# Kernel tuning notes

Hardware: AMD Instinct MI355X
Metric: run time of the kernel (lower is better)

Reference implementation:

```python
import jax, jax.numpy as jnp
import numpy as np

B, N, C_IN, T, K, C_OUT = 16, 1024, 64, 24, 3, 64


def setup_inputs() -> dict:
    key = jax.random.key(0)
    k1, k2, k3, k4 = jax.random.split(key, 4)
    x = jax.random.normal(k1, (B, N, C_IN, T), dtype=jnp.float32)
    STDG = jax.random.uniform(k2, (B, N, N), dtype=jnp.float32)
    cheb = jax.random.normal(k3, (K, N, N), dtype=jnp.float32)
    theta = jax.random.normal(k4, (K, C_IN, C_OUT), dtype=jnp.float32)
    return {"x": x, "STDG": STDG, "cheb": cheb, "theta": theta}


def reference(x, STDG, cheb, theta):
    # x: [B, N, C_in, T]; STDG: [B, N, N]; cheb: [K, N, N]; theta: [K, C_in, C_out]
    # original per (t, k): ((T_k * STDG).T @ x[..., t]) @ theta_k, summed over k, relu
    masked = cheb[:, None, :, :] * STDG[None]              # [K, B, N, N]
    # transpose of masked acts on node dim m: out_n = sum_m masked[k,b,m,n] * x[b,m,c,t]
    rhs = jnp.einsum('kbmn,bmct->kbnct', masked, x)        # [K, B, N, C_in, T]
    out = jnp.einsum('kbnct,kco->bnot', rhs, theta)        # [B, N, C_out, T]
    return jax.nn.relu(out)
```

## Files before the change

kernel.cpp:

```cpp
#include <hip/hip_runtime.h>
#include <stdint.h>


#define BB   16
#define NN   1024
#define CIN  64
#define TT   24
#define KCH  3
#define COUT 64
#define PP   (KCH*NN)
#define JJ   (COUT*TT)

typedef __attribute__((ext_vector_type(4))) float f32x4;
typedef __attribute__((ext_vector_type(8))) short bf16x8;

typedef __attribute__((address_space(1))) const unsigned int* gas_cuintp;
typedef __attribute__((address_space(3))) unsigned int* las_uintp;

static __device__ __forceinline__ unsigned short f2bf(float f){
  union { float f; unsigned u; } v; v.f = f;
  unsigned r = v.u + 0x7fffu + ((v.u >> 16) & 1u);
  return (unsigned short)(r >> 16);
}

__global__ __launch_bounds__(256) void kprepA(const float* __restrict__ cheb,
                                              const float* __restrict__ stdg,
                                              unsigned short* __restrict__ Ah,
                                              int b0){
  int nt = blockIdx.x;
  int mt = blockIdx.y;
  int bk = blockIdx.z;
  int bb = bk / 3, k = bk - bb * 3;
  int b = b0 + bb;
  __shared__ float alds[64][65];
  int tid = threadIdx.x;
  {
    int rm = tid >> 2;
    int nc = (tid & 3) << 4;
    const float* cp = cheb + ((size_t)(k*NN + mt*64 + rm))*NN + nt*64 + nc;
    const float* sp = stdg + ((size_t)(b*NN + mt*64 + rm))*NN + nt*64 + nc;
    #pragma unroll
    for (int i = 0; i < 16; i += 4){
      f32x4 cv = *(const f32x4*)(cp + i);
      f32x4 sv = *(const f32x4*)(sp + i);
      #pragma unroll
      for (int q = 0; q < 4; q++) alds[nc + i + q][rm] = cv[q] * sv[q];
    }
  }
  __syncthreads();
  {
    int rn = tid >> 2;
    int mc = (tid & 3) << 4;
    union { unsigned short s[16]; uint4 v[2]; } hb;
    #pragma unroll
    for (int i = 0; i < 16; i++) hb.s[i] = f2bf(alds[rn][mc + i]);
    size_t ob = ((size_t)(bb*NN + nt*64 + rn))*PP + (size_t)k*NN + mt*64 + mc;
    *(uint4*)(Ah + ob)     = hb.v[0];
    *(uint4*)(Ah + ob + 8) = hb.v[1];
  }
}

__global__ __launch_bounds__(256) void kprepY(const float* __restrict__ x,
                                              const float* __restrict__ theta,
                                              unsigned short* __restrict__ Yt,
                                              int b0){
  int jb = blockIdx.x;
  int ms = blockIdx.y;
  int bb = blockIdx.z;
  int b  = b0 + bb;
  __shared__ float xs[32*196];
  __shared__ float ths[3*64*8];
  __shared__ unsigned short ytile[192*32];
  int tid = threadIdx.x;
  int mi = tid >> 3, oi = tid & 7;

  for (int i = tid; i < 3*64*8; i += 256){
    int k = i >> 9, rem = i & 511;
    int c = rem >> 3, o = rem & 7;
    ths[i] = theta[k*(CIN*COUT) + c*COUT + jb*8 + o];
  }

  float acc0[24], acc1[24], acc2[24];
  #pragma unroll
  for (int t = 0; t < 24; t++){ acc0[t]=0.f; acc1[t]=0.f; acc2[t]=0.f; }

  const f32x4* xg4 = (const f32x4*)(x + ((size_t)(b*NN + ms*32))*CIN*TT);
  for (int cc = 0; cc < 8; cc++){
    __syncthreads();
    for (int i4 = tid; i4 < 32*48; i4 += 256){
      int m = i4 / 48, r = i4 - m*48;
      *(f32x4*)&xs[m*196 + r*4] = xg4[m*384 + cc*48 + r];
    }
    __syncthreads();
    for (int c8 = 0; c8 < 8; c8++){
      float xv[24];
      #pragma unroll
      for (int q = 0; q < 6; q++) *(f32x4*)&xv[q*4] = *(const f32x4*)&xs[mi*196 + c8*24 + q*4];
      int cg = cc*8 + c8;
      float t0 = ths[0*512 + cg*8 + oi];
      float t1 = ths[1*512 + cg*8 + oi];
      float t2 = ths[2*512 + cg*8 + oi];
      #pragma unroll
      for (int t = 0; t < 24; t++){
        acc0[t] = fmaf(t0, xv[t], acc0[t]);
        acc1[t] = fmaf(t1, xv[t], acc1[t]);
        acc2[t] = fmaf(t2, xv[t], acc2[t]);
      }
    }
  }

  #pragma unroll
  for (int k = 0; k < 3; k++){
    const float* a = (k==0) ? acc0 : (k==1) ? acc1 : acc2;
    __syncthreads();
    #pragma unroll
    for (int t = 0; t < 24; t++){
      int row = oi*24 + t;
      int sw  = (row >> 3) & 3;
      int sc  = (mi >> 3) ^ sw;
      ytile[row*32 + sc*8 + (mi & 7)] = f2bf(a[t]);
    }
    __syncthreads();
    for (int r = 0; r < 3; r++){
      int i   = tid + r*256;
      int row = i >> 2, c4 = i & 3;
      int sw  = (row >> 3) & 3;
      uint4 v = *(const uint4*)&ytile[row*32 + (c4 ^ sw)*8];
      size_t ob = ((size_t)bb*JJ + (size_t)jb*192 + row)*PP + k*NN + ms*32 + c4*8;
      *(uint4*)(Yt + ob) = v;
    }
  }
}

__global__ __launch_bounds__(256, 2) void kgemm(
    const unsigned short* __restrict__ Ah,
    const unsigned short* __restrict__ Yh,
    float* __restrict__ out, int b0){
  __shared__ unsigned short AsL[128*64];
  __shared__ unsigned short YsL[128*64];
  int orig = blockIdx.x;
  int cpx  = (int)(gridDim.x >> 3);
  int wgid = ((orig & 7) * cpx) + (orig >> 3);
  int bb  = wgid / 96;
  int r96 = wgid - bb*96;
  int nt  = r96 / 12;
  int jt  = r96 - nt*12;
  int tid = threadIdx.x;
  int lane = tid & 63, wave = tid >> 6;
  int wr = wave >> 1, wc = wave & 1;

  unsigned aoff[4], yoff[4];
  #pragma unroll
  for (int it = 0; it < 4; it++){
    int c = tid + it*256;
    int row = c >> 3;
    int sc = (c & 7) ^ (row & 7);
    aoff[it] = (unsigned)(((bb*NN + nt*128 + row) * PP) * 2 + sc * 16);
    yoff[it] = (unsigned)(((bb*JJ + jt*128 + row) * PP) * 2 + sc * 16);
  }

  f32x4 acc[4][4];
  #pragma unroll
  for (int i = 0; i < 4; i++)
    #pragma unroll
    for (int q = 0; q < 4; q++) acc[i][q] = (f32x4){0.f, 0.f, 0.f, 0.f};

  unsigned ldsw = (unsigned)(wave * 1024);
  const char* pA = (const char*)Ah;
  const char* pY = (const char*)Yh;

  for (int ps = 0; ps < PP/64; ps++){
    unsigned so = (unsigned)(ps * 128);
    #pragma unroll
    for (int it = 0; it < 4; it++){
      unsigned ld = ldsw + it*4096;
      __builtin_amdgcn_global_load_lds((gas_cuintp)(pA + aoff[it] + so), (las_uintp)((char*)AsL + ld), 16, 0, 0);
      __builtin_amdgcn_global_load_lds((gas_cuintp)(pY + yoff[it] + so), (las_uintp)((char*)YsL + ld), 16, 0, 0);
    }
    __syncthreads();
    #pragma unroll
    for (int kk = 0; kk < 2; kk++){
      bf16x8 a_f[4], y_f[4];
      #pragma unroll
      for (int i = 0; i < 4; i++){
        int arow = wr*64 + i*16 + (lane & 15);
        int ach  = ((kk*4) + (lane >> 4)) ^ (arow & 7);
        a_f[i] = *(const bf16x8*)&AsL[arow*64 + ach*8];
        int jrow = wc*64 + i*16 + (lane & 15);
        int jch  = ((kk*4) + (lane >> 4)) ^ (jrow & 7);
        y_f[i] = *(const bf16x8*)&YsL[jrow*64 + jch*8];
      }
      #pragma unroll
      for (int i = 0; i < 4; i++)
        #pragma unroll
        for (int q = 0; q < 4; q++)
          acc[i][q] = __builtin_amdgcn_mfma_f32_16x16x32_bf16(a_f[i], y_f[q], acc[i][q], 0, 0, 0);
    }
    __syncthreads();
  }
  size_t ob = (size_t)(b0 + bb) * NN * JJ;
  #pragma unroll
  for (int i = 0; i < 4; i++){
    int nbase = nt*128 + wr*64 + i*16 + ((lane >> 4) << 2);
    #pragma unroll
    for (int q = 0; q < 4; q++){
      int j = jt*128 + wc*64 + q*16 + (lane & 15);
      #pragma unroll
      for (int e = 0; e < 4; e++){
        float v = acc[i][q][e];
        v = v > 0.f ? v : 0.f;
        out[ob + (size_t)(nbase + e) * JJ + j] = v;
      }
    }
  }
}

extern "C" void kernel_launch(void* const* d_in, const int* in_sizes, int n_in,
                              void* d_out, int out_size, void* d_ws, size_t ws_size,
                              hipStream_t stream){
  (void)in_sizes; (void)n_in; (void)out_size;
  const float* x     = (const float*)d_in[0];
  const float* stdg  = (const float*)d_in[1];
  const float* cheb  = (const float*)d_in[2];
  const float* theta = (const float*)d_in[3];
  float* out = (float*)d_out;

  const size_t szA_b = (size_t)NN * PP * sizeof(unsigned short);
  const size_t szY_b = (size_t)PP * JJ * sizeof(unsigned short);
  const size_t per_b = szA_b + szY_b;
  int NB = 16;
  while (NB > 1 && per_b * (size_t)NB > ws_size) NB >>= 1;

  char* w = (char*)d_ws;
  unsigned short* Ah = (unsigned short*)w;                         w += szA_b * NB;
  unsigned short* Yt = (unsigned short*)w;                         w += szY_b * NB;

  for (int b0 = 0; b0 < BB; b0 += NB){
    kprepA<<<dim3(16, 16, NB*3), 256, 0, stream>>>(cheb, stdg, Ah, b0);
    kprepY<<<dim3(8, 32, NB),    256, 0, stream>>>(x, theta, Yt, b0);
    kgemm<<<dim3(NB*96),         256, 0, stream>>>(Ah, Yt, out, b0);
  }
}
```

Measured before the change: 657.8 us.

## Reuse cheb tiles across batches in A-prep and swap prepY grid axes

The A-prep kernel now loads all three Chebyshev tiles for a node tile into shared memory once. It then loops over every batch in the chunk, multiplying each by that batch's STDG tile, instead of launching a separate block per (batch, k) pair that reloads cheb each time. This is meant to cut redundant global reads of cheb. In exchange, the grid shrinks to 256 large blocks using about 66 KB of LDS, each working through batches sequentially with barriers, so occupancy and latency hiding fall. The Y-prep grid also swaps its x/y axes so consecutive blocks cover different node slices, which changes launch order and cache locality.

```diff
diff --git a/kernel.cpp b/kernel.cpp
--- a/kernel.cpp
+++ b/kernel.cpp
@@ -26,37 +26,46 @@
 __global__ __launch_bounds__(256) void kprepA(const float* __restrict__ cheb,
                                               const float* __restrict__ stdg,
                                               unsigned short* __restrict__ Ah,
-                                              int b0){
+                                              int b0, int nb){
   int nt = blockIdx.x;
   int mt = blockIdx.y;
-  int bk = blockIdx.z;
-  int bb = bk / 3, k = bk - bb * 3;
-  int b = b0 + bb;
-  __shared__ float alds[64][65];
+  __shared__ float ct[3][64][65];
+  __shared__ float st[64][65];
   int tid = threadIdx.x;
-  {
-    int rm = tid >> 2;
-    int nc = (tid & 3) << 4;
+  int rm = tid >> 2;
+  int nc = (tid & 3) << 4;
+  #pragma unroll
+  for (int k = 0; k < 3; k++){
     const float* cp = cheb + ((size_t)(k*NN + mt*64 + rm))*NN + nt*64 + nc;
-    const float* sp = stdg + ((size_t)(b*NN + mt*64 + rm))*NN + nt*64 + nc;
     #pragma unroll
     for (int i = 0; i < 16; i += 4){
       f32x4 cv = *(const f32x4*)(cp + i);
+      #pragma unroll
+      for (int q = 0; q < 4; q++) ct[k][nc + i + q][rm] = cv[q];
+    }
+  }
+  int rn = tid >> 2;
+  int mc = (tid & 3) << 4;
+  for (int bb = 0; bb < nb; bb++){
+    int b = b0 + bb;
+    __syncthreads();
+    const float* sp = stdg + ((size_t)(b*NN + mt*64 + rm))*NN + nt*64 + nc;
+    #pragma unroll
+    for (int i = 0; i < 16; i += 4){
       f32x4 sv = *(const f32x4*)(sp + i);
       #pragma unroll
-      for (int q = 0; q < 4; q++) alds[nc + i + q][rm] = cv[q] * sv[q];
-    }
-  }
-  __syncthreads();
-  {
-    int rn = tid >> 2;
-    int mc = (tid & 3) << 4;
-    union { unsigned short s[16]; uint4 v[2]; } hb;
-    #pragma unroll
-    for (int i = 0; i < 16; i++) hb.s[i] = f2bf(alds[rn][mc + i]);
-    size_t ob = ((size_t)(bb*NN + nt*64 + rn))*PP + (size_t)k*NN + mt*64 + mc;
-    *(uint4*)(Ah + ob)     = hb.v[0];
-    *(uint4*)(Ah + ob + 8) = hb.v[1];
+      for (int q = 0; q < 4; q++) st[nc + i + q][rm] = sv[q];
+    }
+    __syncthreads();
+    #pragma unroll
+    for (int k = 0; k < 3; k++){
+      union { unsigned short s[16]; uint4 v[2]; } hb;
+      #pragma unroll
+      for (int i = 0; i < 16; i++) hb.s[i] = f2bf(ct[k][rn][mc + i] * st[rn][mc + i]);
+      size_t ob = ((size_t)(bb*NN + nt*64 + rn))*PP + (size_t)k*NN + mt*64 + mc;
+      *(uint4*)(Ah + ob)     = hb.v[0];
+      *(uint4*)(Ah + ob + 8) = hb.v[1];
+    }
   }
 }
 
@@ -64,8 +73,8 @@
                                               const float* __restrict__ theta,
                                               unsigned short* __restrict__ Yt,
                                               int b0){
-  int jb = blockIdx.x;
-  int ms = blockIdx.y;
+  int ms = blockIdx.x;
+  int jb = blockIdx.y;
   int bb = blockIdx.z;
   int b  = b0 + bb;
   __shared__ float xs[32*196];
@@ -236,8 +245,8 @@
   unsigned short* Yt = (unsigned short*)w;                         w += szY_b * NB;
 
   for (int b0 = 0; b0 < BB; b0 += NB){
-    kprepA<<<dim3(16, 16, NB*3), 256, 0, stream>>>(cheb, stdg, Ah, b0);
-    kprepY<<<dim3(8, 32, NB),    256, 0, stream>>>(x, theta, Yt, b0);
-    kgemm<<<dim3(NB*96),         256, 0, stream>>>(Ah, Yt, out, b0);
-  }
-}
+    kprepA<<<dim3(16, 16),    256, 0, stream>>>(cheb, stdg, Ah, b0, NB);
+    kprepY<<<dim3(32, 8, NB), 256, 0, stream>>>(x, theta, Yt, b0);
+    kgemm<<<dim3(NB*96),      256, 0, stream>>>(Ah, Yt, out, b0);
+  }
+}
```

New measurement: 659.7 us. About the same (+0.3%).
